# Kernel tuning notes

Measured on AMD Instinct MI355X. Metric: run time of the kernel, lower is better.

The kernel has to match this reference:

```python
import jax, jax.numpy as jnp
import numpy as np

EPS = 1e-12          # sinkhorn_knopp epsilon
LOW, HIGH = 0.02, 0.98  # SquashedSigmoid bounds
N_ITERS = 10         # num_iterations
BATCH = 2097152


def setup_inputs() -> dict:
    key = jax.random.key(0)
    ks = jax.random.split(key, 9)
    dims = [6, 64, 32, 16, 9]
    inp = {"margins": jax.random.uniform(ks[0], (BATCH, 6), jnp.float32, 0.05, 1.0)}
    for i in range(4):
        fi, fo = dims[i], dims[i + 1]
        inp[f"W{i+1}"] = jax.random.normal(ks[1 + 2 * i], (fi, fo), jnp.float32) / np.float32(np.sqrt(fi))
        inp[f"b{i+1}"] = jnp.zeros((fo,), jnp.float32)
    return inp


def _mlp(x, W1, b1, W2, b2, W3, b3, W4, b4):
    h = jax.nn.relu(x @ W1 + b1)
    h = jax.nn.relu(h @ W2 + b2)
    h = jax.nn.relu(h @ W3 + b3)
    return h @ W4 + b4  # [B, 9]


def _tau(p4):
    # user-supplied tau: 4 positive params -> 3x3 matrix; 2x2 block padded with ones
    B = p4.shape[0]
    A = jnp.ones((B, 3, 3), p4.dtype)
    return A.at[:, :2, :2].set(p4.reshape(B, 2, 2))


def _sinkhorn_knopp(A, r, c):
    # batched row/col balancing; per-sample A is 3x3, r/c are length-3 margins
    for _ in range(N_ITERS):
        A = A * (r[:, :, None] / (A.sum(axis=2, keepdims=True) + EPS))
        A = A * (c[:, None, :] / (A.sum(axis=1, keepdims=True) + EPS))
    return A


def reference(margins, W1, b1, W2, b2, W3, b3, W4, b4):
    B = margins.shape[0]
    M, F = margins[:, 0:3], margins[:, 3:6]
    pars = _mlp(margins, W1, b1, W2, b2, W3, b3, W4, b4)
    muc = _tau(jnp.exp(pars[:, 0:4]))                     # [B,3,3]
    sqs = lambda x: LOW + (HIGH - LOW) * jax.nn.sigmoid(x)
    shm, shf = sqs(pars[:, 4:6]), sqs(pars[:, 6:8])
    V = jnp.exp(pars[:, -1])                              # [B]
    ones = jnp.ones((B, 1), margins.dtype)
    shm0 = jnp.concatenate([shm, ones], axis=1)           # [B,3]
    shf0 = jnp.concatenate([shf, ones], axis=1)
    mucm0, muc0f = M * shm0, F * shf0                     # row / col margins
    mum0, mu0f = M * (1 - shm0), F * (1 - shf0)
    muc = _sinkhorn_knopp(muc, mucm0, muc0f)              # [B,3,3]
    top = jnp.concatenate([muc, mum0[:, :, None]], axis=2)                    # [B,3,4]
    bot = jnp.concatenate([mu0f[:, None, :], jnp.zeros((B, 1, 1), margins.dtype)], axis=2)  # [B,1,4]
    mus = jnp.concatenate([top, bot], axis=1)             # [B,4,4]
    return (mus, V)
```

## Files before the change

kernel.cpp:

```cpp
#include <hip/hip_runtime.h>

typedef _Float16 f16x8 __attribute__((ext_vector_type(8)));
typedef float    f32x4 __attribute__((ext_vector_type(4)));

static constexpr float kEPS  = 1e-12f;
static constexpr float kLOW  = 0.02f;
static constexpr float kHIGH = 0.98f;

__device__ __forceinline__ float fast_sigmoid(float v) {
    return 1.0f / (1.0f + __expf(-v));
}

__global__ __launch_bounds__(256, 2) void sinkhorn_mlp_mfma(
    const float* __restrict__ margins,
    const float* __restrict__ W1, const float* __restrict__ b1,
    const float* __restrict__ W2, const float* __restrict__ b2,
    const float* __restrict__ W3, const float* __restrict__ b3,
    const float* __restrict__ W4, const float* __restrict__ b4,
    float* __restrict__ out_mus, float* __restrict__ out_V, int B)
{
    __shared__ __align__(16) char smem_all[4 * 9216];
    const int lane = threadIdx.x & 63;
    const int wid  = threadIdx.x >> 6;
    char* smem = smem_all + wid * 9216;

    const int n16 = lane & 15;
    const int q   = lane >> 4;

    const int row  = blockIdx.x * 256 + wid * 64 + lane;
    const int rowC = row < B ? row : (B - 1);

    f16x8 B2f[2][2];
#pragma unroll
    for (int kt = 0; kt < 2; ++kt)
#pragma unroll
        for (int nt = 0; nt < 2; ++nt)
#pragma unroll
            for (int j = 0; j < 8; ++j)
                B2f[kt][nt][j] = (_Float16)W2[(kt*32 + q*8 + j)*32 + nt*16 + n16];

    f16x8 B3f;
#pragma unroll
    for (int j = 0; j < 8; ++j)
        B3f[j] = (_Float16)W3[(q*8 + j)*16 + n16];

    const float bias2_0 = b2[n16];
    const float bias2_1 = b2[16 + n16];
    const float bias3   = b3[n16];

    float x[6];
    {
        const float* mp = margins + (size_t)rowC * 6;
#pragma unroll
        for (int i = 0; i < 6; ++i) x[i] = mp[i];
    }

    float h1[64];
#pragma unroll
    for (int k = 0; k < 64; ++k) h1[k] = b1[k];
#pragma unroll
    for (int i = 0; i < 6; ++i) {
        const float xi = x[i];
        const float* w = W1 + i * 64;
#pragma unroll
        for (int k = 0; k < 64; ++k) h1[k] = fmaf(xi, w[k], h1[k]);
    }

    {
        char* rp = smem + lane * 144;
#pragma unroll
        for (int i = 0; i < 8; ++i) {
            f16x8 hv;
#pragma unroll
            for (int j = 0; j < 8; ++j)
                hv[j] = (_Float16)fmaxf(h1[8*i + j], 0.0f);
            *(f16x8*)(rp + i * 16) = hv;
        }
    }

    f16x8 A2[4][2];
#pragma unroll
    for (int mt = 0; mt < 4; ++mt)
#pragma unroll
        for (int kt = 0; kt < 2; ++kt)
            A2[mt][kt] = *(const f16x8*)(smem + (mt*16 + n16)*144 + kt*64 + q*16);

#pragma unroll
    for (int mt = 0; mt < 4; ++mt) {
#pragma unroll
        for (int nt = 0; nt < 2; ++nt) {
            f32x4 C;
            const float bb = nt ? bias2_1 : bias2_0;
            C[0] = bb; C[1] = bb; C[2] = bb; C[3] = bb;
            C = __builtin_amdgcn_mfma_f32_16x16x32_f16(A2[mt][0], B2f[0][nt], C, 0, 0, 0);
            C = __builtin_amdgcn_mfma_f32_16x16x32_f16(A2[mt][1], B2f[1][nt], C, 0, 0, 0);
            const int row0 = mt*16 + q*4;
            char* base = smem + (size_t)(nt*16 + n16) * 2;
#pragma unroll
            for (int r = 0; r < 4; ++r)
                *(_Float16*)(base + (row0 + r) * 80) = (_Float16)fmaxf(C[r], 0.0f);
        }
    }

    f16x8 A3[4];
#pragma unroll
    for (int mt = 0; mt < 4; ++mt)
        A3[mt] = *(const f16x8*)(smem + (mt*16 + n16)*80 + q*16);

#pragma unroll
    for (int mt = 0; mt < 4; ++mt) {
        f32x4 C;
        C[0] = bias3; C[1] = bias3; C[2] = bias3; C[3] = bias3;
        C = __builtin_amdgcn_mfma_f32_16x16x32_f16(A3[mt], B3f, C, 0, 0, 0);
        const int row0 = mt*16 + q*4;
#pragma unroll
        for (int r = 0; r < 4; ++r)
            *(float*)(smem + (row0 + r) * 80 + n16 * 4) = fmaxf(C[r], 0.0f);
    }

    float h3[16];
    {
        const char* rp = smem + lane * 80;
#pragma unroll
        for (int i = 0; i < 4; ++i)
            *(f32x4*)&h3[4*i] = *(const f32x4*)(rp + i * 16);
    }

    float p[9];
#pragma unroll
    for (int k = 0; k < 9; ++k) p[k] = b4[k];
#pragma unroll
    for (int j = 0; j < 16; ++j) {
        const float hj = h3[j];
        const float* w = W4 + j * 9;
#pragma unroll
        for (int k = 0; k < 9; ++k) p[k] = fmaf(hj, w[k], p[k]);
    }

    float A00 = __expf(p[0]), A01 = __expf(p[1]);
    float A10 = __expf(p[2]), A11 = __expf(p[3]);
    float A02 = 1.0f, A12 = 1.0f, A20 = 1.0f, A21 = 1.0f, A22 = 1.0f;

    const float sh_m0 = kLOW + (kHIGH - kLOW) * fast_sigmoid(p[4]);
    const float sh_m1 = kLOW + (kHIGH - kLOW) * fast_sigmoid(p[5]);
    const float sh_f0 = kLOW + (kHIGH - kLOW) * fast_sigmoid(p[6]);
    const float sh_f1 = kLOW + (kHIGH - kLOW) * fast_sigmoid(p[7]);
    const float V = __expf(p[8]);

    const float M0 = x[0], M1 = x[1], M2 = x[2];
    const float F0 = x[3], F1 = x[4], F2 = x[5];

    const float r0 = M0 * sh_m0, r1 = M1 * sh_m1, r2 = M2;
    const float c0 = F0 * sh_f0, c1 = F1 * sh_f1, c2 = F2;
    const float mum0_0 = M0 * (1.0f - sh_m0), mum0_1 = M1 * (1.0f - sh_m1);
    const float mu0f_0 = F0 * (1.0f - sh_f0), mu0f_1 = F1 * (1.0f - sh_f1);

#pragma unroll
    for (int it = 0; it < 10; ++it) {
        float s0 = A00 + A01 + A02;
        float s1 = A10 + A11 + A12;
        float s2 = A20 + A21 + A22;
        float f0 = __fdividef(r0, s0 + kEPS);
        float f1 = __fdividef(r1, s1 + kEPS);
        float f2 = __fdividef(r2, s2 + kEPS);
        A00 *= f0; A01 *= f0; A02 *= f0;
        A10 *= f1; A11 *= f1; A12 *= f1;
        A20 *= f2; A21 *= f2; A22 *= f2;
        float t0 = A00 + A10 + A20;
        float t1 = A01 + A11 + A21;
        float t2 = A02 + A12 + A22;
        float g0 = __fdividef(c0, t0 + kEPS);
        float g1 = __fdividef(c1, t1 + kEPS);
        float g2 = __fdividef(c2, t2 + kEPS);
        A00 *= g0; A10 *= g0; A20 *= g0;
        A01 *= g1; A11 *= g1; A21 *= g1;
        A02 *= g2; A12 *= g2; A22 *= g2;
    }

    if (row < B) {
        float4* o = (float4*)(out_mus + (size_t)row * 16);
        o[0] = make_float4(A00, A01, A02, mum0_0);
        o[1] = make_float4(A10, A11, A12, mum0_1);
        o[2] = make_float4(A20, A21, A22, 0.0f);
        o[3] = make_float4(mu0f_0, mu0f_1, 0.0f, 0.0f);
        out_V[row] = V;
    }
}

extern "C" void kernel_launch(void* const* d_in, const int* in_sizes, int n_in,
                              void* d_out, int out_size, void* d_ws, size_t ws_size,
                              hipStream_t stream) {
    const float* margins = (const float*)d_in[0];
    const float* W1 = (const float*)d_in[1];
    const float* b1 = (const float*)d_in[2];
    const float* W2 = (const float*)d_in[3];
    const float* b2 = (const float*)d_in[4];
    const float* W3 = (const float*)d_in[5];
    const float* b3 = (const float*)d_in[6];
    const float* W4 = (const float*)d_in[7];
    const float* b4 = (const float*)d_in[8];

    const int B = in_sizes[0] / 6;
    float* out_mus = (float*)d_out;
    float* out_V   = out_mus + (size_t)B * 16;

    dim3 block(256);
    dim3 grid((B + 255) / 256);
    hipLaunchKernelGGL(sinkhorn_mlp_mfma, grid, block, 0, stream,
                       margins, W1, b1, W2, b2, W3, b3, W4, b4,
                       out_mus, out_V, B);
}
```

Measured before the change: 250.7 us.

## Reformulate Sinkhorn as u/v scaling vectors and cut register pressure for occupancy

Replaces the per-iteration 3x3 matrix rescaling with the equivalent dual form that tracks row and column scaling vectors u and v and only forms the matrix at the end. It also drops the epsilon and uses hardware reciprocal. Layer 1 is computed per output column straight into the fp16 staging buffer instead of holding a 64-float accumulator array, and launch bounds rise from 2 to 4 blocks per SM. The intent is fewer ALU ops and registers for higher occupancy, at the risk of small numeric drift from removing epsilon and reordering the arithmetic.

```diff
diff --git a/kernel.cpp b/kernel.cpp
--- a/kernel.cpp
+++ b/kernel.cpp
@@ -3,15 +3,17 @@
 typedef _Float16 f16x8 __attribute__((ext_vector_type(8)));
 typedef float    f32x4 __attribute__((ext_vector_type(4)));
 
-static constexpr float kEPS  = 1e-12f;
 static constexpr float kLOW  = 0.02f;
 static constexpr float kHIGH = 0.98f;
 
 __device__ __forceinline__ float fast_sigmoid(float v) {
     return 1.0f / (1.0f + __expf(-v));
 }
-
-__global__ __launch_bounds__(256, 2) void sinkhorn_mlp_mfma(
+__device__ __forceinline__ float fast_rcp(float v) {
+    return __builtin_amdgcn_rcpf(v);
+}
+
+__global__ __launch_bounds__(256, 4) void sinkhorn_mlp_mfma(
     const float* __restrict__ margins,
     const float* __restrict__ W1, const float* __restrict__ b1,
     const float* __restrict__ W2, const float* __restrict__ b2,
@@ -55,26 +57,20 @@
         for (int i = 0; i < 6; ++i) x[i] = mp[i];
     }
 
-    float h1[64];
-#pragma unroll
-    for (int k = 0; k < 64; ++k) h1[k] = b1[k];
-#pragma unroll
-    for (int i = 0; i < 6; ++i) {
-        const float xi = x[i];
-        const float* w = W1 + i * 64;
-#pragma unroll
-        for (int k = 0; k < 64; ++k) h1[k] = fmaf(xi, w[k], h1[k]);
-    }
-
     {
         char* rp = smem + lane * 144;
 #pragma unroll
-        for (int i = 0; i < 8; ++i) {
+        for (int c = 0; c < 8; ++c) {
             f16x8 hv;
 #pragma unroll
-            for (int j = 0; j < 8; ++j)
-                hv[j] = (_Float16)fmaxf(h1[8*i + j], 0.0f);
-            *(f16x8*)(rp + i * 16) = hv;
+            for (int k = 0; k < 8; ++k) {
+                const int col = c * 8 + k;
+                float a = fmaf(x[0], W1[col], b1[col]);
+#pragma unroll
+                for (int i = 1; i < 6; ++i) a = fmaf(x[i], W1[i * 64 + col], a);
+                hv[k] = (_Float16)fmaxf(a, 0.0f);
+            }
+            *(f16x8*)(rp + c * 16) = hv;
         }
     }
 
@@ -128,18 +124,17 @@
 
     float p[9];
 #pragma unroll
-    for (int k = 0; k < 9; ++k) p[k] = b4[k];
-#pragma unroll
-    for (int j = 0; j < 16; ++j) {
+    for (int k = 0; k < 9; ++k) p[k] = fmaf(h3[0], W4[k], b4[k]);
+#pragma unroll
+    for (int j = 1; j < 16; ++j) {
         const float hj = h3[j];
         const float* w = W4 + j * 9;
 #pragma unroll
         for (int k = 0; k < 9; ++k) p[k] = fmaf(hj, w[k], p[k]);
     }
 
-    float A00 = __expf(p[0]), A01 = __expf(p[1]);
-    float A10 = __expf(p[2]), A11 = __expf(p[3]);
-    float A02 = 1.0f, A12 = 1.0f, A20 = 1.0f, A21 = 1.0f, A22 = 1.0f;
+    const float K00 = __expf(p[0]), K01 = __expf(p[1]);
+    const float K10 = __expf(p[2]), K11 = __expf(p[3]);
 
     const float sh_m0 = kLOW + (kHIGH - kLOW) * fast_sigmoid(p[4]);
     const float sh_m1 = kLOW + (kHIGH - kLOW) * fast_sigmoid(p[5]);
@@ -155,27 +150,26 @@
     const float mum0_0 = M0 * (1.0f - sh_m0), mum0_1 = M1 * (1.0f - sh_m1);
     const float mu0f_0 = F0 * (1.0f - sh_f0), mu0f_1 = F1 * (1.0f - sh_f1);
 
+    float u0, u1, u2;
+    float v0 = 1.0f, v1 = 1.0f, v2 = 1.0f;
 #pragma unroll
     for (int it = 0; it < 10; ++it) {
-        float s0 = A00 + A01 + A02;
-        float s1 = A10 + A11 + A12;
-        float s2 = A20 + A21 + A22;
-        float f0 = __fdividef(r0, s0 + kEPS);
-        float f1 = __fdividef(r1, s1 + kEPS);
-        float f2 = __fdividef(r2, s2 + kEPS);
-        A00 *= f0; A01 *= f0; A02 *= f0;
-        A10 *= f1; A11 *= f1; A12 *= f1;
-        A20 *= f2; A21 *= f2; A22 *= f2;
-        float t0 = A00 + A10 + A20;
-        float t1 = A01 + A11 + A21;
-        float t2 = A02 + A12 + A22;
-        float g0 = __fdividef(c0, t0 + kEPS);
-        float g1 = __fdividef(c1, t1 + kEPS);
-        float g2 = __fdividef(c2, t2 + kEPS);
-        A00 *= g0; A10 *= g0; A20 *= g0;
-        A01 *= g1; A11 *= g1; A21 *= g1;
-        A02 *= g2; A12 *= g2; A22 *= g2;
-    }
+        const float s0 = fmaf(K00, v0, fmaf(K01, v1, v2));
+        const float s1 = fmaf(K10, v0, fmaf(K11, v1, v2));
+        const float s2 = v0 + v1 + v2;
+        u0 = r0 * fast_rcp(s0);
+        u1 = r1 * fast_rcp(s1);
+        u2 = r2 * fast_rcp(s2);
+        const float t0 = fmaf(K00, u0, fmaf(K10, u1, u2));
+        const float t1 = fmaf(K01, u0, fmaf(K11, u1, u2));
+        const float t2 = u0 + u1 + u2;
+        v0 = c0 * fast_rcp(t0);
+        v1 = c1 * fast_rcp(t1);
+        v2 = c2 * fast_rcp(t2);
+    }
+    const float A00 = u0 * K00 * v0, A01 = u0 * K01 * v1, A02 = u0 * v2;
+    const float A10 = u1 * K10 * v0, A11 = u1 * K11 * v1, A12 = u1 * v2;
+    const float A20 = u2 * v0,       A21 = u2 * v1,       A22 = u2 * v2;
 
     if (row < B) {
         float4* o = (float4*)(out_mus + (size_t)row * 16);
```

Result: faster. 229.9 us (-8.3%).
